# Kernel optimization log

Measured on AMD Instinct MI355X. Metric: run time of the kernel, lower is better.

## Reference

```python
import jax, jax.numpy as jnp
import numpy as np

T, B, D, H = 512, 64, 1024, 1024


def setup_inputs() -> dict:
    key = jax.random.key(0)
    k_x, k_wi, k_wh = jax.random.split(key, 3)
    scale_i = 1.0 / np.sqrt(D)
    scale_h = 1.0 / np.sqrt(H)
    return {
        "x": jax.random.normal(k_x, (T, B, D), dtype=jnp.float32),
        "c0": jnp.zeros((B, H), dtype=jnp.float32),
        "h0": jnp.zeros((B, H), dtype=jnp.float32),
        "Wi": jax.random.normal(k_wi, (D, 4 * H), dtype=jnp.float32) * scale_i,
        "Wh": jax.random.normal(k_wh, (H, 4 * H), dtype=jnp.float32) * scale_h,
        "b": jnp.zeros((4 * H,), dtype=jnp.float32),
    }


def reference(x, c0, h0, Wi, Wh, b):
    """LSTM recurrence over leading (time) axis, faithful to flax LSTMCell math.

    Gates: i = sigmoid, f = sigmoid, g = tanh, o = sigmoid;
    c' = f*c + i*g; h' = o*tanh(c'). Input projection has no bias, hidden
    projection carries the bias (matching flax LSTMCell). Returns ys = h per
    step, shape [T, B, H] (the scan outputs of the original module).
    """
    # Precompute the input-side gate projection for all timesteps at once
    # (one big GEMM instead of T small ones): [T, B, 4H]
    xg = jnp.einsum("tbd,dg->tbg", x, Wi)

    hdim = Wh.shape[0]

    def step(carry, xg_t):
        c, h = carry
        gates = xg_t + h @ Wh + b  # [B, 4H]
        i, f, g, o = jnp.split(gates, 4, axis=-1)
        i = jax.nn.sigmoid(i)
        f = jax.nn.sigmoid(f)
        g = jnp.tanh(g)
        o = jax.nn.sigmoid(o)
        c_new = f * c + i * g
        h_new = o * jnp.tanh(c_new)
        return (c_new, h_new), h_new

    (_, _), ys = jax.lax.scan(step, (c0, h0), xg)
    return ys  # [T, B, H]
```

## Files before the change

### kernel.cpp

```cpp
#include <hip/hip_runtime.h>
#include <hip/hip_bf16.h>


#define T_STEPS  512
#define BATCH    64
#define DIM      1024
#define NG       4096
#define NBLK     256
#define PTHREADS 512
#define NGRP     4
#define GBLK     64
#define GB       16
#define HSLOT    ((size_t)(BATCH * DIM + 2048))

typedef __attribute__((ext_vector_type(8))) short frag8;
typedef __attribute__((ext_vector_type(4))) float f32x4;

__device__ __forceinline__ short f2bf(float f) {
    union { float f; unsigned u; } v; v.f = f;
    unsigned r = v.u + 0x7fffu + ((v.u >> 16) & 1u);
    return (short)(r >> 16);
}
__device__ __forceinline__ float sigm(float x) { return 1.0f / (1.0f + __expf(-x)); }
__device__ __forceinline__ float tanh_fast(float x) { return 1.0f - 2.0f / (__expf(2.0f * x) + 1.0f); }


__global__ __launch_bounds__(256)
void cast_transpose(const float* __restrict__ W, short* __restrict__ WT) {
    __shared__ float tile[32][33];
    int k0 = blockIdx.x * 32;
    int n0 = blockIdx.y * 32;
    int tx = threadIdx.x & 31, ty = threadIdx.x >> 5;
    #pragma unroll
    for (int i = 0; i < 32; i += 8)
        tile[ty + i][tx] = W[(size_t)(k0 + ty + i) * NG + n0 + tx];
    __syncthreads();
    #pragma unroll
    for (int i = 0; i < 32; i += 8)
        WT[(size_t)(n0 + ty + i) * DIM + k0 + tx] = f2bf(tile[tx][ty + i]);
}

__global__ __launch_bounds__(256)
void init_state(const float* __restrict__ c0, const float* __restrict__ h0,
                float* __restrict__ c, short* __restrict__ hring,
                unsigned* __restrict__ flags) {
    int i = blockIdx.x * 256 + threadIdx.x;
    c[i] = c0[i];
    hring[i] = f2bf(h0[i]);
    if (i < NBLK * 32) flags[i] = 0u;
}

__global__ __launch_bounds__(256)
void xcast(const float* __restrict__ x, short* __restrict__ xb, int n8) {
    int i = blockIdx.x * 256 + threadIdx.x;
    if (i >= n8) return;
    const float4* p = (const float4*)(x + (size_t)i * 8);
    float4 a = p[0], b = p[1];
    frag8 v;
    v[0] = f2bf(a.x); v[1] = f2bf(a.y); v[2] = f2bf(a.z); v[3] = f2bf(a.w);
    v[4] = f2bf(b.x); v[5] = f2bf(b.y); v[6] = f2bf(b.z); v[7] = f2bf(b.w);
    *(frag8*)(xb + (size_t)i * 8) = v;
}

__global__ __launch_bounds__(256)
void xgemm(const short* __restrict__ A, const short* __restrict__ B,
           float* __restrict__ CT_, int M) {
    __shared__ short As[4096];
    __shared__ short Bs[4096];
    const int tid = threadIdx.x;
    const int w = tid >> 6, l = tid & 63, m = l & 15, q = l >> 4;
    const size_t abase = (size_t)blockIdx.x * 128 * DIM;
    const size_t bbase = (size_t)blockIdx.y * 128 * DIM;

    f32x4 acc[2][8];
    #pragma unroll
    for (int i = 0; i < 2; ++i)
        #pragma unroll
        for (int j = 0; j < 8; ++j) acc[i][j] = (f32x4){0.f, 0.f, 0.f, 0.f};

    for (int kc = 0; kc < 32; ++kc) {
        #pragma unroll
        for (int c2 = 0; c2 < 2; ++c2) {
            int t2 = c2 * 256 + tid;
            int seg = t2 >> 7, row = t2 & 127;
            const short* ga = A + abase + (size_t)row * DIM + kc * 32 + seg * 8;
            const short* gb = B + bbase + (size_t)row * DIM + kc * 32 + seg * 8;
            __builtin_amdgcn_global_load_lds(
                (const __attribute__((address_space(1))) void*)ga,
                (__attribute__((address_space(3))) void*)(As + t2 * 8), 16, 0, 0);
            __builtin_amdgcn_global_load_lds(
                (const __attribute__((address_space(1))) void*)gb,
                (__attribute__((address_space(3))) void*)(Bs + t2 * 8), 16, 0, 0);
        }
        __syncthreads();
        frag8 a0 = *(const frag8*)(As + (q * 128 + w * 32 + m) * 8);
        frag8 a1 = *(const frag8*)(As + (q * 128 + w * 32 + 16 + m) * 8);
        #pragma unroll
        for (int nt = 0; nt < 8; ++nt) {
            frag8 bf = *(const frag8*)(Bs + (q * 128 + nt * 16 + m) * 8);
            acc[0][nt] = __builtin_amdgcn_mfma_f32_16x16x32_bf16(a0, bf, acc[0][nt], 0, 0, 0);
            acc[1][nt] = __builtin_amdgcn_mfma_f32_16x16x32_bf16(a1, bf, acc[1][nt], 0, 0, 0);
        }
        __syncthreads();
    }
    #pragma unroll
    for (int mt = 0; mt < 2; ++mt)
        #pragma unroll
        for (int nt = 0; nt < 8; ++nt) {
            int row0 = blockIdx.x * 128 + w * 32 + mt * 16 + q * 4;
            int col  = blockIdx.y * 128 + nt * 16 + m;
            *(float4*)(CT_ + (size_t)col * M + row0) =
                make_float4(acc[mt][nt][0], acc[mt][nt][1], acc[mt][nt][2], acc[mt][nt][3]);
        }
}

__global__ __launch_bounds__(PTHREADS, 1)
void lstm_persist(const float* __restrict__ xgT,
                  const short* __restrict__ WhT,
                  const float* __restrict__ bias,
                  float* __restrict__ cstate,
                  short* __restrict__ hring,
                  float* __restrict__ y,
                  unsigned* __restrict__ flags,
                  int gstep0, int CTC, int M) {
    __shared__ short whs[4 * 32 * 64 * 8];
    __shared__ float gsm2[2][16][68];
    const int tid = threadIdx.x;
    const int w = tid >> 6, l = tid & 63, m = l & 15, q4 = l >> 4;
    const int cg = w & 3, kh = w >> 2;
    const int grp  = blockIdx.x >> 6;
    const int kblk = blockIdx.x & 63;
    const int j0   = kblk * 16;

    for (int idx = tid; idx < 4 * 32 * 64; idx += PTHREADS) {
        int scg = idx >> 11, rem = idx & 2047;
        int kcc = rem >> 6, ll = rem & 63, cc = ll & 15, qq = ll >> 4;
        int gcol = (cc >> 2) * DIM + j0 + scg * 4 + (cc & 3);
        *(frag8*)(whs + idx * 8) =
            *(const frag8*)(WhT + (size_t)gcol * DIM + kcc * 32 + qq * 8);
    }

    const int bl = l & 15;
    const int jl = w * 4 + q4;
    const int eb = grp * GB + bl;
    const int ec = j0 + jl;
    float creg = 0.f, bv0 = 0.f, bv1 = 0.f, bv2 = 0.f, bv3 = 0.f;
    if (tid < 256) {
        creg = cstate[(size_t)eb * DIM + ec];
        bv0 = bias[0 * DIM + ec];
        bv1 = bias[1 * DIM + ec];
        bv2 = bias[2 * DIM + ec];
        bv3 = bias[3 * DIM + ec];
    }
    __syncthreads();

    for (int t = 0; t < CTC; ++t) {
        float xv0 = 0.f, xv1 = 0.f, xv2 = 0.f, xv3 = 0.f;
        if (tid < 256) {
            const size_t r = (size_t)t * BATCH + eb;
            xv0 = xgT[(size_t)(0 * DIM + ec) * M + r];
            xv1 = xgT[(size_t)(1 * DIM + ec) * M + r];
            xv2 = xgT[(size_t)(2 * DIM + ec) * M + r];
            xv3 = xgT[(size_t)(3 * DIM + ec) * M + r];
        }

        if (t > 0 && w == 0) {
            const unsigned target = (unsigned)(gstep0 + t);
            const unsigned* fp = &flags[(grp * GBLK + l) * 32];
            for (;;) {
                unsigned f = __hip_atomic_load(fp, __ATOMIC_RELAXED,
                                               __HIP_MEMORY_SCOPE_AGENT);
                if (__all(f >= target)) break;
                __builtin_amdgcn_s_sleep(1);
            }
        }
        __syncthreads();

        const short* hrow = hring + (size_t)t * HSLOT
                          + (size_t)(grp * GB + m) * DIM + kh * 512;
        f32x4 acc = {0.f, 0.f, 0.f, 0.f};
        #pragma unroll
        for (int kc = 0; kc < 16; ++kc) {
            frag8 a = *(const frag8*)(hrow + kc * 32 + q4 * 8);
            frag8 b = *(const frag8*)(whs + ((cg * 32 + kh * 16 + kc) * 64 + l) * 8);
            acc = __builtin_amdgcn_mfma_f32_16x16x32_bf16(a, b, acc, 0, 0, 0);
        }
        #pragma unroll
        for (int r = 0; r < 4; ++r)
            gsm2[kh][q4 * 4 + r][(m >> 2) * 16 + cg * 4 + (m & 3)] = acc[r];
        __syncthreads();

        float hn = 0.f, ya = 0.f, yb = 0.f, yc = 0.f;
        unsigned long long hv = 0ull;
        if (tid < 256) {
            const float gi = sigm(     gsm2[0][bl][ 0 + jl] + gsm2[1][bl][ 0 + jl] + xv0 + bv0);
            const float gf = sigm(     gsm2[0][bl][16 + jl] + gsm2[1][bl][16 + jl] + xv1 + bv1);
            const float gg = tanh_fast(gsm2[0][bl][32 + jl] + gsm2[1][bl][32 + jl] + xv2 + bv2);
            const float go = sigm(     gsm2[0][bl][48 + jl] + gsm2[1][bl][48 + jl] + xv3 + bv3);
            creg = gf * creg + gi * gg;
            hn = go * tanh_fast(creg);

            ya = __shfl(hn, bl + 16);
            yb = __shfl(hn, bl + 32);
            yc = __shfl(hn, bl + 48);
            unsigned hb0 = (unsigned)(unsigned short)f2bf(hn);
            unsigned hb1 = __shfl(hb0, bl + 16);
            unsigned hb2 = __shfl(hb0, bl + 32);
            unsigned hb3 = __shfl(hb0, bl + 48);
            if (l < 16) {
                const int dslot = (t == CTC - 1) ? 0 : (t + 1);
                hv = (unsigned long long)(hb0 | (hb1 << 16))
                   | ((unsigned long long)(hb2 | (hb3 << 16)) << 32);
                __hip_atomic_store(
                    (unsigned long long*)(hring + (size_t)dslot * HSLOT
                                          + (size_t)eb * DIM + j0 + w * 4),
                    hv, __ATOMIC_RELAXED, __HIP_MEMORY_SCOPE_AGENT);
            }
        }

        if (t < CTC - 1) {
            asm volatile("s_waitcnt vmcnt(0)" ::: "memory");
            __syncthreads();
            if (tid == 0)
                __hip_atomic_store(&flags[blockIdx.x * 32], (unsigned)(gstep0 + t + 1),
                                   __ATOMIC_RELAXED, __HIP_MEMORY_SCOPE_AGENT);
        }

        if (tid < 256 && l < 16)
            *(float4*)(y + ((size_t)t * BATCH + eb) * DIM + j0 + w * 4) =
                make_float4(hn, ya, yb, yc);
    }
    if (tid < 256) cstate[(size_t)eb * DIM + ec] = creg;
}

extern "C" void kernel_launch(void* const* d_in, const int* in_sizes, int n_in,
                              void* d_out, int out_size, void* d_ws, size_t ws_size,
                              hipStream_t stream) {
    const float* x  = (const float*)d_in[0];
    const float* c0 = (const float*)d_in[1];
    const float* h0 = (const float*)d_in[2];
    const float* Wi = (const float*)d_in[3];
    const float* Wh = (const float*)d_in[4];
    const float* b  = (const float*)d_in[5];
    float* out = (float*)d_out;

    char* ws = (char*)d_ws;
    short*    WiT   = (short*)(ws);
    short*    WhT   = (short*)(ws + 8388608);
    float*    c     = (float*)(ws + 16777216);
    unsigned* flags = (unsigned*)(ws + 17039360);
    const size_t fixed = 17072128;

    const size_t perCT = HSLOT * 2 + 131072 + 1048576;
    int CT = 2;
    const int cands[9] = {512, 256, 128, 64, 32, 16, 8, 4, 2};
    for (int i = 0; i < 9; ++i)
        if (fixed + (size_t)cands[i] * perCT <= ws_size) { CT = cands[i]; break; }

    short* hring = (short*)(ws + fixed);
    short* xbf   = (short*)(ws + fixed + (size_t)CT * HSLOT * 2);
    float* xgT   = (float*)(ws + fixed + (size_t)CT * (HSLOT * 2 + 131072));
    const int M = CT * BATCH;

    cast_transpose<<<dim3(DIM / 32, NG / 32), 256, 0, stream>>>(Wi, WiT);
    cast_transpose<<<dim3(DIM / 32, NG / 32), 256, 0, stream>>>(Wh, WhT);
    init_state<<<dim3(BATCH * DIM / 256), 256, 0, stream>>>(c0, h0, c, hring, flags);

    const int nchunks = T_STEPS / CT;
    for (int ch = 0; ch < nchunks; ++ch) {
        const size_t xoff = (size_t)ch * CT * BATCH * DIM;
        const int n8 = CT * BATCH * DIM / 8;
        xcast<<<dim3((n8 + 255) / 256), 256, 0, stream>>>(x + xoff, xbf, n8);
        xgemm<<<dim3(M / 128, NG / 128), 256, 0, stream>>>(xbf, WiT, xgT, M);
        lstm_persist<<<dim3(NBLK), PTHREADS, 0, stream>>>(
            xgT, WhT, b, c, hring, out + xoff, flags, ch * CT, CT, M);
    }
}
```

Before: 4.130 ms.

## Use per-wave completion flags to drop block barrier before signaling

Each of the four gate-computing waves now publishes its own progress flag once its hidden-state store has drained, replacing the block-wide barrier followed by a single flag write. Consumers poll four flags per producer block. The change also transposes the gate scratch buffer to reduce LDS bank conflicts, prefetches the next step's input projection into cache from an otherwise idle wave, and writes outputs with nontemporal stores. These remove a barrier from the serial critical path at the cost of four times more flag traffic while polling.

```diff
diff --git a/kernel.cpp b/kernel.cpp
--- a/kernel.cpp
+++ b/kernel.cpp
@@ -47,7 +47,7 @@
     int i = blockIdx.x * 256 + threadIdx.x;
     c[i] = c0[i];
     hring[i] = f2bf(h0[i]);
-    if (i < NBLK * 32) flags[i] = 0u;
+    if (i < NBLK * 4 * 32) flags[i] = 0u;
 }
 
 __global__ __launch_bounds__(256)
@@ -124,7 +124,7 @@
                   unsigned* __restrict__ flags,
                   int gstep0, int CTC, int M) {
     __shared__ short whs[4 * 32 * 64 * 8];
-    __shared__ float gsm2[2][16][68];
+    __shared__ float gsm2[2][64][17];
     const int tid = threadIdx.x;
     const int w = tid >> 6, l = tid & 63, m = l & 15, q4 = l >> 4;
     const int cg = w & 3, kh = w >> 2;
@@ -166,11 +166,19 @@
 
         if (t > 0 && w == 0) {
             const unsigned target = (unsigned)(gstep0 + t);
-            const unsigned* fp = &flags[(grp * GBLK + l) * 32];
+            const unsigned* fp = &flags[((grp * GBLK + l) * 4) * 32];
             for (;;) {
-                unsigned f = __hip_atomic_load(fp, __ATOMIC_RELAXED,
-                                               __HIP_MEMORY_SCOPE_AGENT);
-                if (__all(f >= target)) break;
+                unsigned f0 = __hip_atomic_load(fp +  0, __ATOMIC_RELAXED,
+                                                __HIP_MEMORY_SCOPE_AGENT);
+                unsigned f1 = __hip_atomic_load(fp + 32, __ATOMIC_RELAXED,
+                                                __HIP_MEMORY_SCOPE_AGENT);
+                unsigned f2 = __hip_atomic_load(fp + 64, __ATOMIC_RELAXED,
+                                                __HIP_MEMORY_SCOPE_AGENT);
+                unsigned f3 = __hip_atomic_load(fp + 96, __ATOMIC_RELAXED,
+                                                __HIP_MEMORY_SCOPE_AGENT);
+                bool ok = (f0 >= target) & (f1 >= target)
+                        & (f2 >= target) & (f3 >= target);
+                if (__all(ok)) break;
                 __builtin_amdgcn_s_sleep(1);
             }
         }
@@ -187,48 +195,55 @@
         }
         #pragma unroll
         for (int r = 0; r < 4; ++r)
-            gsm2[kh][q4 * 4 + r][(m >> 2) * 16 + cg * 4 + (m & 3)] = acc[r];
-        __syncthreads();
-
-        float hn = 0.f, ya = 0.f, yb = 0.f, yc = 0.f;
-        unsigned long long hv = 0ull;
+            gsm2[kh][(m >> 2) * 16 + cg * 4 + (m & 3)][q4 * 4 + r] = acc[r];
+        __syncthreads();
+
+        if (w == 4 && t + 1 < CTC) {
+            const int g = l >> 4, ecp = j0 + (l & 15);
+            float pf = xgT[(size_t)(g * DIM + ecp) * M
+                           + (size_t)(t + 1) * BATCH + grp * GB];
+            asm volatile("" :: "v"(pf));
+        }
+
         if (tid < 256) {
-            const float gi = sigm(     gsm2[0][bl][ 0 + jl] + gsm2[1][bl][ 0 + jl] + xv0 + bv0);
-            const float gf = sigm(     gsm2[0][bl][16 + jl] + gsm2[1][bl][16 + jl] + xv1 + bv1);
-            const float gg = tanh_fast(gsm2[0][bl][32 + jl] + gsm2[1][bl][32 + jl] + xv2 + bv2);
-            const float go = sigm(     gsm2[0][bl][48 + jl] + gsm2[1][bl][48 + jl] + xv3 + bv3);
+            const float gi = sigm(     gsm2[0][ 0 + jl][bl] + gsm2[1][ 0 + jl][bl] + xv0 + bv0);
+            const float gf = sigm(     gsm2[0][16 + jl][bl] + gsm2[1][16 + jl][bl] + xv1 + bv1);
+            const float gg = tanh_fast(gsm2[0][32 + jl][bl] + gsm2[1][32 + jl][bl] + xv2 + bv2);
+            const float go = sigm(     gsm2[0][48 + jl][bl] + gsm2[1][48 + jl][bl] + xv3 + bv3);
             creg = gf * creg + gi * gg;
-            hn = go * tanh_fast(creg);
-
-            ya = __shfl(hn, bl + 16);
-            yb = __shfl(hn, bl + 32);
-            yc = __shfl(hn, bl + 48);
+            const float hn = go * tanh_fast(creg);
+
+            const float ya = __shfl(hn, bl + 16);
+            const float yb = __shfl(hn, bl + 32);
+            const float yc = __shfl(hn, bl + 48);
             unsigned hb0 = (unsigned)(unsigned short)f2bf(hn);
             unsigned hb1 = __shfl(hb0, bl + 16);
             unsigned hb2 = __shfl(hb0, bl + 32);
             unsigned hb3 = __shfl(hb0, bl + 48);
             if (l < 16) {
                 const int dslot = (t == CTC - 1) ? 0 : (t + 1);
-                hv = (unsigned long long)(hb0 | (hb1 << 16))
-                   | ((unsigned long long)(hb2 | (hb3 << 16)) << 32);
+                unsigned long long hv = (unsigned long long)(hb0 | (hb1 << 16))
+                                      | ((unsigned long long)(hb2 | (hb3 << 16)) << 32);
                 __hip_atomic_store(
                     (unsigned long long*)(hring + (size_t)dslot * HSLOT
                                           + (size_t)eb * DIM + j0 + w * 4),
                     hv, __ATOMIC_RELAXED, __HIP_MEMORY_SCOPE_AGENT);
             }
-        }
-
-        if (t < CTC - 1) {
-            asm volatile("s_waitcnt vmcnt(0)" ::: "memory");
-            __syncthreads();
-            if (tid == 0)
-                __hip_atomic_store(&flags[blockIdx.x * 32], (unsigned)(gstep0 + t + 1),
-                                   __ATOMIC_RELAXED, __HIP_MEMORY_SCOPE_AGENT);
-        }
-
-        if (tid < 256 && l < 16)
-            *(float4*)(y + ((size_t)t * BATCH + eb) * DIM + j0 + w * 4) =
-                make_float4(hn, ya, yb, yc);
+
+            if (t < CTC - 1) {
+                asm volatile("s_waitcnt vmcnt(0)" ::: "memory");
+                if (l == 0)
+                    __hip_atomic_store(&flags[(blockIdx.x * 4 + w) * 32],
+                                       (unsigned)(gstep0 + t + 1),
+                                       __ATOMIC_RELAXED, __HIP_MEMORY_SCOPE_AGENT);
+            }
+
+            if (l < 16) {
+                f32x4 yv; yv[0] = hn; yv[1] = ya; yv[2] = yb; yv[3] = yc;
+                __builtin_nontemporal_store(
+                    yv, (f32x4*)(y + ((size_t)t * BATCH + eb) * DIM + j0 + w * 4));
+            }
+        }
     }
     if (tid < 256) cstate[(size_t)eb * DIM + ec] = creg;
 }
@@ -249,7 +264,7 @@
     short*    WhT   = (short*)(ws + 8388608);
     float*    c     = (float*)(ws + 16777216);
     unsigned* flags = (unsigned*)(ws + 17039360);
-    const size_t fixed = 17072128;
+    const size_t fixed = 17170432;
 
     const size_t perCT = HSLOT * 2 + 131072 + 1048576;
     int CT = 2;
```

Result: slower. 4.266 ms (+3.3%).
